# Optimization experiments

Measured on AMD Instinct MI355X. Metric: run time of the kernel, lower is better.

## Reference

```python
import jax, jax.numpy as jnp
import numpy as np

N_PIX = 65536   # 256x256 render
N_GAUSS = 2048
N_COL = 3


def setup_inputs() -> dict:
    key = jax.random.key(0)
    k1, k2, k3, k4 = jax.random.split(key, 4)
    x = jax.random.uniform(k1, (N_PIX, 2), dtype=jnp.float32)           # pixel coords
    mus = jax.random.uniform(k2, (N_GAUSS, 2), dtype=jnp.float32)       # Gaussian means
    # SPD covariances: A A^T + sigma*I  (small spatial extent ~0.05)
    A = jax.random.normal(k3, (N_GAUSS, 2, 2), dtype=jnp.float32) * 0.05
    covs = jnp.einsum('mij,mkj->mik', A, A) + 0.01 * jnp.eye(2, dtype=jnp.float32)
    cols = jax.random.uniform(k4, (N_GAUSS, N_COL), dtype=jnp.float32)  # RGB per Gaussian
    return {"x": x, "mus": mus, "covs": covs, "cols": cols}


def reference(x, mus, covs, cols):
    # d: [N, M, 2] pixel-to-mean offsets
    d = x[:, None, :] - mus[None, :, :]
    # solve(covs, d) per (pixel, Gaussian) == cov_inv @ d; covs depend only on Gaussian,
    # so invert once per Gaussian (same math as torch.linalg.solve per pair).
    cov_inv = jnp.linalg.inv(covs)                      # [M, 2, 2]
    maha = jnp.einsum('nmi,mij,nmj->nm', d, cov_inv, d)  # [N, M] Mahalanobis distances
    w = jnp.exp(-0.5 * maha)                             # [N, M] Gaussian weights
    # weighted sum of colors over Gaussians: [N, M] @ [M, 3] -> [N, 3]
    return jnp.einsum('nm,mc->nc', w, cols)
```

## Files before the change

kernel.cpp:

```cpp
#include <hip/hip_runtime.h>

#define N_PIX   65536
#define N_GAUSS 2048

typedef __bf16 bf16x8 __attribute__((ext_vector_type(8)));
typedef float  f32x4  __attribute__((ext_vector_type(4)));

union BF8U { uint4 u; bf16x8 h; };
__device__ inline bf16x8 as_bf(uint4 u) { BF8U x; x.u = u; return x.h; }

__device__ inline unsigned short bfbits(float f) {
  __bf16 h = (__bf16)f;
  return __builtin_bit_cast(unsigned short, h);
}
__device__ inline float bf2f(unsigned short b) {
  return (float)__builtin_bit_cast(__bf16, b);
}
__device__ inline unsigned pkb(unsigned short a, unsigned short b) {
  return (unsigned)a | ((unsigned)b << 16);
}
__device__ inline unsigned pk2f(float a, float b) {
  return pkb(bfbits(a), bfbits(b));
}


__global__ __launch_bounds__(256) void prep_kernel(
    const float* __restrict__ mus, const float* __restrict__ covs,
    const float* __restrict__ cols, uint4* __restrict__ ws) {
  int tid = blockIdx.x * 256 + threadIdx.x;
  if (tid < 8192) {
    int lane = tid & 63;
    int tile = tid >> 6;
    int grp  = lane >> 4;
    int g    = tile * 16 + (lane & 15);
    float c00 = covs[4*g+0], c01 = covs[4*g+1];
    float c10 = covs[4*g+2], c11 = covs[4*g+3];
    float inv_det = 1.0f / (c00*c11 - c01*c10);
    float ia =  c11 * inv_det;
    float ib = -c01 * inv_det;
    float ic =  c00 * inv_det;
    float mx = mus[2*g+0], my = mus[2*g+1];
    const float kk = -0.7213475204444817f;
    float coef[6];
    coef[0] = kk * ia;
    coef[1] = kk * 2.0f * ib;
    coef[2] = kk * ic;
    coef[3] = -2.0f * kk * (ia*mx + ib*my);
    coef[4] = -2.0f * kk * (ib*mx + ic*my);
    coef[5] = kk * (ia*mx*mx + 2.0f*ib*mx*my + ic*my*my);
    unsigned short ch[6], cl[6];
    #pragma unroll
    for (int i = 0; i < 6; ++i) {
      ch[i] = bfbits(coef[i]);
      cl[i] = bfbits(coef[i] - bf2f(ch[i]));
    }
    uint4 v = make_uint4(0,0,0,0);
    if (grp == 0)      v = make_uint4(pkb(ch[0],ch[1]), pkb(ch[2],ch[3]), pkb(ch[4],ch[5]), pkb(cl[0],cl[1]));
    else if (grp == 1) v = make_uint4(pkb(cl[2],cl[3]), pkb(cl[4],cl[5]), pkb(ch[0],ch[1]), pkb(ch[2],ch[3]));
    else if (grp == 2) v = make_uint4(pkb(ch[4],ch[5]), pkb(cl[0],cl[1]), pkb(cl[2],cl[3]), pkb(cl[4],cl[5]));
    ws[tid] = v;
  } else if (tid < 12288) {
    int t2   = tid - 8192;
    int lane = t2 & 63;
    int tile = t2 >> 6;
    int rgb  = lane & 15;
    int grp  = lane >> 4;
    uint4 v = make_uint4(0,0,0,0);
    if (rgb < 3) {
      unsigned short b[8];
      #pragma unroll
      for (int j = 0; j < 8; ++j) {
        int sig = 4*grp + (j & 3) + ((j >> 2) ? 16 : 0);
        b[j] = bfbits(cols[(tile*32 + sig)*3 + rgb]);
      }
      v = make_uint4(pkb(b[0],b[1]), pkb(b[2],b[3]), pkb(b[4],b[5]), pkb(b[6],b[7]));
    }
    ws[8192 + t2] = v;
  }
}

__global__ __launch_bounds__(512, 4) void render_kernel(
    const float2* __restrict__ x, const uint4* __restrict__ ws,
    float* __restrict__ out) {
  __shared__ uint4 smem[1024];
  const uint4* gq  = ws;
  const uint4* pvc = ws + 8192;

  int tid  = threadIdx.x;
  int lane = tid & 63;
  int c    = lane & 15, grp = lane >> 4;
  int wave = tid >> 6;
  int wpix = blockIdx.x * 128 + wave * 16;

  float2 p = x[wpix + c];
  float mono[6] = {p.x*p.x, p.x*p.y, p.y*p.y, p.x, p.y, 1.0f};
  unsigned short ph[6], pl[6];
  #pragma unroll
  for (int i = 0; i < 6; ++i) {
    ph[i] = bfbits(mono[i]);
    pl[i] = bfbits(mono[i] - bf2f(ph[i]));
  }
  uint4 pv4 = make_uint4(0,0,0,0);
  if (grp == 0)      pv4 = make_uint4(pkb(ph[0],ph[1]), pkb(ph[2],ph[3]), pkb(ph[4],ph[5]), pkb(ph[0],ph[1]));
  else if (grp == 1) pv4 = make_uint4(pkb(ph[2],ph[3]), pkb(ph[4],ph[5]), pkb(pl[0],pl[1]), pkb(pl[2],pl[3]));
  else if (grp == 2) pv4 = make_uint4(pkb(pl[4],pl[5]), pkb(pl[0],pl[1]), pkb(pl[2],pl[3]), pkb(pl[4],pl[5]));
  bf16x8 pf = as_bf(pv4);

  f32x4 acc  = {0.f, 0.f, 0.f, 0.f};
  const f32x4 zero = {0.f, 0.f, 0.f, 0.f};

  uint4 s0 = gq[tid], s1 = gq[512 + tid];
  for (int chk = 0; chk < 8; ++chk) {
    __syncthreads();
    smem[tid] = s0; smem[512 + tid] = s1;
    __syncthreads();
    if (chk < 7) {
      s0 = gq[(chk+1)*1024 + tid];
      s1 = gq[(chk+1)*1024 + 512 + tid];
    }
    uint4 cf[8];
    #pragma unroll
    for (int t = 0; t < 8; ++t)
      cf[t] = pvc[chk*512 + t*64 + lane];
    #pragma unroll
    for (int pr = 0; pr < 8; ++pr) {
      uint4 ga = smem[(2*pr+0)*64 + lane];
      uint4 gb = smem[(2*pr+1)*64 + lane];
      f32x4 q0 = __builtin_amdgcn_mfma_f32_16x16x32_bf16(as_bf(ga), pf, zero, 0, 0, 0);
      f32x4 q1 = __builtin_amdgcn_mfma_f32_16x16x32_bf16(as_bf(gb), pf, zero, 0, 0, 0);
      unsigned w0 = pk2f(__builtin_amdgcn_exp2f(q0[0]), __builtin_amdgcn_exp2f(q0[1]));
      unsigned w1 = pk2f(__builtin_amdgcn_exp2f(q0[2]), __builtin_amdgcn_exp2f(q0[3]));
      unsigned w2 = pk2f(__builtin_amdgcn_exp2f(q1[0]), __builtin_amdgcn_exp2f(q1[1]));
      unsigned w3 = pk2f(__builtin_amdgcn_exp2f(q1[2]), __builtin_amdgcn_exp2f(q1[3]));
      uint4 wf = make_uint4(w0, w1, w2, w3);
      acc = __builtin_amdgcn_mfma_f32_16x16x32_bf16(as_bf(cf[pr]), as_bf(wf), acc, 0, 0, 0);
    }
  }
  if (grp == 0) {
    int pix = wpix + c;
    out[pix*3 + 0] = acc[0];
    out[pix*3 + 1] = acc[1];
    out[pix*3 + 2] = acc[2];
  }
}

extern "C" void kernel_launch(void* const* d_in, const int* in_sizes, int n_in,
                              void* d_out, int out_size, void* d_ws, size_t ws_size,
                              hipStream_t stream) {
  const float* x    = (const float*)d_in[0];
  const float* mus  = (const float*)d_in[1];
  const float* covs = (const float*)d_in[2];
  const float* cols = (const float*)d_in[3];
  float* out = (float*)d_out;
  uint4* ws  = (uint4*)d_ws;

  prep_kernel<<<48, 256, 0, stream>>>(mus, covs, cols, ws);
  render_kernel<<<512, 512, 0, stream>>>((const float2*)x, ws, out);
}
```

Measured before the change: 82.16 us.

## Split Gaussians across two blocks and process two pixel tiles per wave

Each wave now handles 32 pixels (two 16-pixel MFMA tiles), so every shared-memory Gaussian coefficient fragment and color fragment feeds two tiles. The Gaussian range is split in half across block pairs to keep the grid size unchanged. Partial results are combined with float atomic adds into an output zeroed by a memset beforehand. This cuts LDS and global coefficient traffic per pixel. In exchange it adds a memset launch, atomic traffic, and a nondeterministic summation order.

```diff
diff --git a/kernel.cpp b/kernel.cpp
--- a/kernel.cpp
+++ b/kernel.cpp
@@ -79,6 +79,33 @@
   }
 }
 
+__device__ inline bf16x8 make_pf(float2 p, int grp) {
+  float mono[6] = {p.x*p.x, p.x*p.y, p.y*p.y, p.x, p.y, 1.0f};
+  unsigned short ph[6], pl[6];
+  #pragma unroll
+  for (int i = 0; i < 6; ++i) {
+    ph[i] = bfbits(mono[i]);
+    pl[i] = bfbits(mono[i] - bf2f(ph[i]));
+  }
+  uint4 v = make_uint4(0,0,0,0);
+  if (grp == 0)      v = make_uint4(pkb(ph[0],ph[1]), pkb(ph[2],ph[3]), pkb(ph[4],ph[5]), pkb(ph[0],ph[1]));
+  else if (grp == 1) v = make_uint4(pkb(ph[2],ph[3]), pkb(ph[4],ph[5]), pkb(pl[0],pl[1]), pkb(pl[2],pl[3]));
+  else if (grp == 2) v = make_uint4(pkb(pl[4],pl[5]), pkb(pl[0],pl[1]), pkb(pl[2],pl[3]), pkb(pl[4],pl[5]));
+  return as_bf(v);
+}
+
+__device__ inline f32x4 step_tile(uint4 ga, uint4 gb, bf16x8 pf, uint4 cf, f32x4 acc) {
+  const f32x4 zero = {0.f, 0.f, 0.f, 0.f};
+  f32x4 q0 = __builtin_amdgcn_mfma_f32_16x16x32_bf16(as_bf(ga), pf, zero, 0, 0, 0);
+  f32x4 q1 = __builtin_amdgcn_mfma_f32_16x16x32_bf16(as_bf(gb), pf, zero, 0, 0, 0);
+  unsigned w0 = pk2f(__builtin_amdgcn_exp2f(q0[0]), __builtin_amdgcn_exp2f(q0[1]));
+  unsigned w1 = pk2f(__builtin_amdgcn_exp2f(q0[2]), __builtin_amdgcn_exp2f(q0[3]));
+  unsigned w2 = pk2f(__builtin_amdgcn_exp2f(q1[0]), __builtin_amdgcn_exp2f(q1[1]));
+  unsigned w3 = pk2f(__builtin_amdgcn_exp2f(q1[2]), __builtin_amdgcn_exp2f(q1[3]));
+  uint4 wf = make_uint4(w0, w1, w2, w3);
+  return __builtin_amdgcn_mfma_f32_16x16x32_bf16(as_bf(cf), as_bf(wf), acc, 0, 0, 0);
+}
+
 __global__ __launch_bounds__(512, 4) void render_kernel(
     const float2* __restrict__ x, const uint4* __restrict__ ws,
     float* __restrict__ out) {
@@ -90,57 +117,46 @@
   int lane = tid & 63;
   int c    = lane & 15, grp = lane >> 4;
   int wave = tid >> 6;
-  int wpix = blockIdx.x * 128 + wave * 16;
+  int pixblk = blockIdx.x & 255;
+  int half   = blockIdx.x >> 8;
+  int cbase  = half * 4;
+  int wpix = pixblk * 256 + wave * 32;
 
-  float2 p = x[wpix + c];
-  float mono[6] = {p.x*p.x, p.x*p.y, p.y*p.y, p.x, p.y, 1.0f};
-  unsigned short ph[6], pl[6];
-  #pragma unroll
-  for (int i = 0; i < 6; ++i) {
-    ph[i] = bfbits(mono[i]);
-    pl[i] = bfbits(mono[i] - bf2f(ph[i]));
-  }
-  uint4 pv4 = make_uint4(0,0,0,0);
-  if (grp == 0)      pv4 = make_uint4(pkb(ph[0],ph[1]), pkb(ph[2],ph[3]), pkb(ph[4],ph[5]), pkb(ph[0],ph[1]));
-  else if (grp == 1) pv4 = make_uint4(pkb(ph[2],ph[3]), pkb(ph[4],ph[5]), pkb(pl[0],pl[1]), pkb(pl[2],pl[3]));
-  else if (grp == 2) pv4 = make_uint4(pkb(pl[4],pl[5]), pkb(pl[0],pl[1]), pkb(pl[2],pl[3]), pkb(pl[4],pl[5]));
-  bf16x8 pf = as_bf(pv4);
+  bf16x8 pf0 = make_pf(x[wpix + c],      grp);
+  bf16x8 pf1 = make_pf(x[wpix + 16 + c], grp);
 
-  f32x4 acc  = {0.f, 0.f, 0.f, 0.f};
-  const f32x4 zero = {0.f, 0.f, 0.f, 0.f};
+  f32x4 acc0 = {0.f, 0.f, 0.f, 0.f};
+  f32x4 acc1 = {0.f, 0.f, 0.f, 0.f};
 
-  uint4 s0 = gq[tid], s1 = gq[512 + tid];
-  for (int chk = 0; chk < 8; ++chk) {
+  uint4 s0 = gq[cbase*1024 + tid], s1 = gq[cbase*1024 + 512 + tid];
+  for (int chk = 0; chk < 4; ++chk) {
     __syncthreads();
     smem[tid] = s0; smem[512 + tid] = s1;
     __syncthreads();
-    if (chk < 7) {
-      s0 = gq[(chk+1)*1024 + tid];
-      s1 = gq[(chk+1)*1024 + 512 + tid];
+    if (chk < 3) {
+      s0 = gq[(cbase+chk+1)*1024 + tid];
+      s1 = gq[(cbase+chk+1)*1024 + 512 + tid];
     }
     uint4 cf[8];
     #pragma unroll
     for (int t = 0; t < 8; ++t)
-      cf[t] = pvc[chk*512 + t*64 + lane];
+      cf[t] = pvc[(cbase+chk)*512 + t*64 + lane];
     #pragma unroll
     for (int pr = 0; pr < 8; ++pr) {
       uint4 ga = smem[(2*pr+0)*64 + lane];
       uint4 gb = smem[(2*pr+1)*64 + lane];
-      f32x4 q0 = __builtin_amdgcn_mfma_f32_16x16x32_bf16(as_bf(ga), pf, zero, 0, 0, 0);
-      f32x4 q1 = __builtin_amdgcn_mfma_f32_16x16x32_bf16(as_bf(gb), pf, zero, 0, 0, 0);
-      unsigned w0 = pk2f(__builtin_amdgcn_exp2f(q0[0]), __builtin_amdgcn_exp2f(q0[1]));
-      unsigned w1 = pk2f(__builtin_amdgcn_exp2f(q0[2]), __builtin_amdgcn_exp2f(q0[3]));
-      unsigned w2 = pk2f(__builtin_amdgcn_exp2f(q1[0]), __builtin_amdgcn_exp2f(q1[1]));
-      unsigned w3 = pk2f(__builtin_amdgcn_exp2f(q1[2]), __builtin_amdgcn_exp2f(q1[3]));
-      uint4 wf = make_uint4(w0, w1, w2, w3);
-      acc = __builtin_amdgcn_mfma_f32_16x16x32_bf16(as_bf(cf[pr]), as_bf(wf), acc, 0, 0, 0);
+      acc0 = step_tile(ga, gb, pf0, cf[pr], acc0);
+      acc1 = step_tile(ga, gb, pf1, cf[pr], acc1);
     }
   }
   if (grp == 0) {
-    int pix = wpix + c;
-    out[pix*3 + 0] = acc[0];
-    out[pix*3 + 1] = acc[1];
-    out[pix*3 + 2] = acc[2];
+    int p0 = wpix + c, p1 = wpix + 16 + c;
+    unsafeAtomicAdd(&out[p0*3 + 0], acc0[0]);
+    unsafeAtomicAdd(&out[p0*3 + 1], acc0[1]);
+    unsafeAtomicAdd(&out[p0*3 + 2], acc0[2]);
+    unsafeAtomicAdd(&out[p1*3 + 0], acc1[0]);
+    unsafeAtomicAdd(&out[p1*3 + 1], acc1[1]);
+    unsafeAtomicAdd(&out[p1*3 + 2], acc1[2]);
   }
 }
 
@@ -154,6 +170,8 @@
   float* out = (float*)d_out;
   uint4* ws  = (uint4*)d_ws;
 
+  hipMemsetAsync(out, 0, (size_t)out_size * sizeof(float), stream);
+
   prep_kernel<<<48, 256, 0, stream>>>(mus, covs, cols, ws);
   render_kernel<<<512, 512, 0, stream>>>((const float2*)x, ws, out);
 }
```

Result: no change. 83.27 us (+1.4%).
